# Kernel optimization log

Measured on AMD Instinct MI355X. Metric: run time of the kernel, lower is better.

The kernel has to match this reference:

```python
import jax, jax.numpy as jnp
import numpy as np

N_NODES = 100000
N_EDGES = 1600000
IN_DIM = 128
HIDDEN = 128


def setup_inputs() -> dict:
    key = jax.random.key(0)
    k1, k2, k3, k4 = jax.random.split(key, 4)
    x = jax.random.normal(k1, (N_NODES, IN_DIM), dtype=jnp.float32)
    edge_index = jax.random.randint(k2, (2, N_EDGES), 0, N_NODES, dtype=jnp.int32)
    # Glorot-ish scale (module zero-inits weights, which would give trivial
    # outputs; use random weights for a meaningful correctness baseline).
    W1 = jax.random.normal(k3, (IN_DIM, HIDDEN), dtype=jnp.float32) * (1.0 / np.sqrt(IN_DIM))
    W2 = jax.random.normal(k4, (HIDDEN, HIDDEN), dtype=jnp.float32) * (1.0 / np.sqrt(HIDDEN))
    return {"x": x, "edge_index": edge_index, "W1": W1, "W2": W2}


def _gcn_conv(h, W, src, dst, norm):
    # linear transform then normalized scatter-add aggregation (PyG GCNConv, bias=False)
    h = h @ W                              # [N, H]
    msg = h[src] * norm[:, None]           # gather + scale: [E+N, H]
    return jax.ops.segment_sum(msg, dst, num_segments=N_NODES)


def reference(x, edge_index, W1, W2):
    # add self-loops
    loops = jnp.arange(N_NODES, dtype=edge_index.dtype)
    src = jnp.concatenate([edge_index[0], loops])
    dst = jnp.concatenate([edge_index[1], loops])
    # symmetric normalization D^{-1/2} (A+I) D^{-1/2}; deg >= 1 due to self-loops
    deg = jax.ops.segment_sum(jnp.ones_like(dst, dtype=x.dtype), dst, num_segments=N_NODES)
    dinv = jax.lax.rsqrt(deg)
    norm = dinv[src] * dinv[dst]           # [E+N]

    h = _gcn_conv(x, W1, src, dst, norm)
    h = jax.nn.relu(h)                     # dropout is identity in eval mode
    h = _gcn_conv(h, W2, src, dst, norm)
    return h
```

## Files before the change

kernel.cpp:

```cpp
#include <hip/hip_runtime.h>
#include <hip/hip_bf16.h>

typedef unsigned short u16;
typedef unsigned int   u32;

typedef __attribute__((ext_vector_type(8))) short short8;
typedef __attribute__((ext_vector_type(4))) float floatx4;

#define HD __device__ __forceinline__

HD float bf16_lo(u32 u) { union { u32 i; float f; } v; v.i = u << 16; return v.f; }
HD float bf16_hi(u32 u) { union { u32 i; float f; } v; v.i = u & 0xffff0000u; return v.f; }
HD u16 f2bf(float f) {
    __hip_bfloat16 h = __float2bfloat16(f);
    u16 s; __builtin_memcpy(&s, &h, 2); return s;
}

#define NPB   256
#define MAXNB 512
#define CH    4096
#define CAP   5120

__global__ void k_wprep(const u32* __restrict__ xw,
                        const void* __restrict__ W1, const void* __restrict__ W2,
                        u16* __restrict__ W1t, u16* __restrict__ W2t,
                        int* __restrict__ flag, int* __restrict__ gbcursor) {
    __shared__ int cnt;
    if (threadIdx.x == 0) cnt = 0;
    __syncthreads();
    int sane = 0;
    for (int i = threadIdx.x; i < 4096; i += 256) {
        u32 v = xw[i];
        int e = (v >> 7) & 0xFF;
        sane += (e >= 107 && e <= 147) ? 1 : 0;
    }
    atomicAdd(&cnt, sane);
    __syncthreads();
    int isbf = (cnt > 2048) ? 1 : 0;
    if (blockIdx.x == 0) {
        if (threadIdx.x == 0) *flag = isbf;
        for (int i = threadIdx.x; i <= MAXNB; i += 256) gbcursor[i] = i * CAP;
    }
    int i = blockIdx.x * blockDim.x + threadIdx.x;
    int w = i >> 14;
    int r = (i >> 7) & 127;
    int c = i & 127;
    const void* W = w ? W2 : W1;
    u16*       Wt = w ? W2t : W1t;
    u16 val;
    if (isbf) val = ((const u16*)W)[c * 128 + r];
    else      val = f2bf(((const float*)W)[c * 128 + r]);
    Wt[r * 128 + c] = val;
}

template <int MODE>
__device__ __forceinline__
void gemm_body(u16* __restrict__ lw, u16* __restrict__ st_all,
               const void* __restrict__ inp, const u16* __restrict__ Wt,
               u16* __restrict__ outb, int ntiles, int isbf, int gw, int nw) {
    int lane = threadIdx.x & 63;
    int wid  = threadIdx.x >> 6;
    int m = lane & 15, q = lane >> 4;
    u16* st = st_all + wid * (16 * 136);

    {
        int r = threadIdx.x >> 1;
        int h = threadIdx.x & 1;
        const short8* src = (const short8*)(Wt + r * 128 + h * 64);
#pragma unroll
        for (int jj = 0; jj < 8; jj++) {
            int slot = h * 8 + jj;
            *(short8*)&lw[r * 128 + ((slot ^ (r & 7)) << 3)] = src[jj];
        }
    }
    __syncthreads();

    for (int t = gw; t < ntiles; t += nw) {
        long r0 = (long)t * 32;
        floatx4 acc[2][8];
#pragma unroll
        for (int g = 0; g < 2; g++)
#pragma unroll
            for (int nt = 0; nt < 8; nt++) acc[g][nt] = (floatx4)0.0f;

        short8 a[2][4];
        if (MODE == 1 || isbf) {
#pragma unroll
            for (int g = 0; g < 2; g++)
#pragma unroll
                for (int kk = 0; kk < 4; kk++)
                    a[g][kk] = *(const short8*)((const u16*)inp +
                                 (r0 + g * 16 + m) * 128 + kk * 32 + q * 8);
        } else {
#pragma unroll
            for (int g = 0; g < 2; g++)
#pragma unroll
                for (int kk = 0; kk < 4; kk++) {
                    const float4* fp = (const float4*)((const float*)inp +
                                 (r0 + g * 16 + m) * 128 + kk * 32 + q * 8);
                    float4 f0 = fp[0], f1 = fp[1];
                    short8 v;
                    v[0] = (short)f2bf(f0.x); v[1] = (short)f2bf(f0.y);
                    v[2] = (short)f2bf(f0.z); v[3] = (short)f2bf(f0.w);
                    v[4] = (short)f2bf(f1.x); v[5] = (short)f2bf(f1.y);
                    v[6] = (short)f2bf(f1.z); v[7] = (short)f2bf(f1.w);
                    a[g][kk] = v;
                }
        }

#pragma unroll
        for (int kk = 0; kk < 4; kk++) {
#pragma unroll
            for (int nt = 0; nt < 8; nt++) {
                int slot = kk * 4 + q;
                short8 b = *(const short8*)&lw[(nt * 16 + m) * 128 +
                                               ((slot ^ (m & 7)) << 3)];
                acc[0][nt] = __builtin_amdgcn_mfma_f32_16x16x32_bf16(a[0][kk], b, acc[0][nt], 0, 0, 0);
                acc[1][nt] = __builtin_amdgcn_mfma_f32_16x16x32_bf16(a[1][kk], b, acc[1][nt], 0, 0, 0);
            }
        }

#pragma unroll
        for (int g = 0; g < 2; g++) {
#pragma unroll
            for (int nt = 0; nt < 8; nt++)
#pragma unroll
                for (int i = 0; i < 4; i++)
                    st[(q * 4 + i) * 136 + nt * 16 + m] = f2bf(acc[g][nt][i]);
            __builtin_amdgcn_s_waitcnt(0);
            u16* gbase = outb + (size_t)(r0 + g * 16) * 128;
#pragma unroll
            for (int j = 0; j < 4; j++) {
                int e   = lane * 8 + j * 512;
                int row = e >> 7, colu = e & 127;
                short8 vv = *(const short8*)&st[row * 136 + colu];
                *(short8*)(gbase + e) = vv;
            }
            __builtin_amdgcn_s_waitcnt(0);
        }
    }
}

__device__ __forceinline__
void coarse_body(char* smem, const int* __restrict__ ei, int* __restrict__ gbcursor,
                 int2* __restrict__ pairs, int E, int chunk) {
    int*  hist = (int*)smem;
    int*  gs   = hist + MAXNB;
    int*  dlt  = gs + MAXNB;
    int*  lofs = dlt + MAXNB;
    int2* lp   = (int2*)(smem + 8192);
    u16*  pb   = (u16*)(smem + 8192 + CH * 8);
    const int* srcp = ei;
    const int* dstp = ei + E;
    int base = chunk * CH;
    int cnt  = min(CH, E - base);

    for (int i = threadIdx.x; i < MAXNB; i += 256) hist[i] = 0;
    __syncthreads();

    int2 e[16];
    int nb_ = 0;
#pragma unroll
    for (int j = 0; j < 16; j++) {
        int i = base + threadIdx.x + j * 256;
        if (i < E) {
            e[j].x = srcp[i];
            e[j].y = dstp[i];
            atomicAdd(&hist[e[j].y >> 8], 1);
            nb_ = j + 1;
        }
    }
    __syncthreads();

    if (threadIdx.x < 64) {
        int lane = threadIdx.x;
        int carry = 0;
#pragma unroll
        for (int t = 0; t < MAXNB / 64; t++) {
            int i = t * 64 + lane;
            int v = hist[i];
            int x = v;
#pragma unroll
            for (int off = 1; off < 64; off <<= 1) {
                int y = __shfl_up(x, off);
                if (lane >= off) x += y;
            }
            gs[i] = carry + x - v;
            carry += __shfl(x, 63);
        }
    }
    __syncthreads();

    for (int b = threadIdx.x; b < MAXNB; b += 256) {
        int c = hist[b];
        lofs[b] = gs[b];
        if (c > 0) {
            int gbase = atomicAdd(&gbcursor[b], c);
            dlt[b] = gbase - gs[b];
        }
    }
    __syncthreads();

    for (int j = 0; j < nb_; j++) {
        int b = e[j].y >> 8;
        int p = atomicAdd(&lofs[b], 1);
        lp[p] = e[j];
        pb[p] = (u16)b;
    }
    __syncthreads();

    for (int p = threadIdx.x; p < cnt; p += 256) {
        pairs[p + dlt[pb[p]]] = lp[p];
    }
}

__global__ void __launch_bounds__(256)
k_fused1(const void* __restrict__ x, const u16* __restrict__ W1t,
         u16* __restrict__ Hb, int ntiles, const int* __restrict__ flagp,
         const int* __restrict__ ei, int* __restrict__ gbcursor,
         int2* __restrict__ pairs, int E, int gemmBlocks) {
    __shared__ __align__(16) char smem[50176];
    if (blockIdx.x < gemmBlocks) {
        int isbf = *flagp;
        int gw = (blockIdx.x * 256 + threadIdx.x) >> 6;
        int nw = gemmBlocks * 4;
        gemm_body<0>((u16*)smem, (u16*)(smem + 32768), x, W1t, Hb, ntiles, isbf, gw, nw);
    } else {
        coarse_body(smem, ei, gbcursor, pairs, E, blockIdx.x - gemmBlocks);
    }
}

__global__ void __launch_bounds__(256)
k_gemm2(const void* __restrict__ inp, const u16* __restrict__ Wt,
        u16* __restrict__ outb, int ntiles) {
    __shared__ u16 lw[128 * 128];
    __shared__ u16 stage[4][16 * 136];
    int gw = (blockIdx.x * 256 + threadIdx.x) >> 6;
    int nw = (gridDim.x * 256) >> 6;
    gemm_body<1>(lw, &stage[0][0], inp, Wt, outb, ntiles, 1, gw, nw);
}

__global__ void __launch_bounds__(256)
k_bucket(const int2* __restrict__ pairs, const int* __restrict__ gbcursor,
         float* __restrict__ dinv, int* __restrict__ rbeg, int* __restrict__ rend,
         int* __restrict__ col, int N) {
    __shared__ int lc[NPB];
    __shared__ int lcur[NPB];
    __shared__ int ws[4];
    __shared__ int wsoff[4];
    int b = blockIdx.x;
    int nbase = b * NPB;
    int tid = threadIdx.x, lane = tid & 63, wid = tid >> 6;
    lc[tid] = 0;
    __syncthreads();
    int p0 = b * CAP, p1 = gbcursor[b];
    for (int p = p0 + tid; p < p1; p += 256)
        atomicAdd(&lc[pairs[p].y - nbase], 1);
    __syncthreads();
    int v = lc[tid];
    int node = nbase + tid;
    if (node < N) dinv[node] = rsqrtf((float)v + 1.0f);
    int x = v;
#pragma unroll
    for (int off = 1; off < 64; off <<= 1) {
        int y = __shfl_up(x, off);
        if (lane >= off) x += y;
    }
    if (lane == 63) ws[wid] = x;
    __syncthreads();
    if (tid == 0) {
        int s = 0;
#pragma unroll
        for (int k2 = 0; k2 < 4; k2++) { wsoff[k2] = s; s += ws[k2]; }
    }
    __syncthreads();
    int excl = p0 + wsoff[wid] + (x - v);
    if (node < N) { rbeg[node] = excl; rend[node] = excl + v; }
    lcur[tid] = excl;
    __syncthreads();
    for (int p = p0 + tid; p < p1; p += 256) {
        int2 e = pairs[p];
        int pos = atomicAdd(&lcur[e.y - nbase], 1);
        col[pos] = e.x;
    }
}

template <int MODE>
__global__ void k_csr_agg(const u16* __restrict__ Hb, const int* __restrict__ col,
                          const int* __restrict__ rbeg, const int* __restrict__ rend,
                          const float* __restrict__ dinv,
                          void* __restrict__ outp, int N, const int* __restrict__ flagp) {
    int isbf = MODE ? *flagp : 1;
    int gw   = (blockIdx.x * blockDim.x + threadIdx.x) >> 6;
    int nw   = (gridDim.x * blockDim.x) >> 6;
    int lane = threadIdx.x & 63;
    const u16* hbl = Hb + lane * 2;
    for (int n = gw; n < N; n += nw) {
        int r0 = rbeg[n], r1 = rend[n];
        float di = dinv[n];
        u32 h = *(const u32*)(hbl + (size_t)n * 128);
        float a0 = bf16_lo(h) * di, a1 = bf16_hi(h) * di;

        for (int base = r0; base < r1; base += 64) {
            int cnt = min(64, r1 - base);
            int   myc = (lane < cnt) ? col[base + lane] : 0;
            float mdv = (lane < cnt) ? dinv[myc] : 0.0f;
            int e = 0;
            for (; e + 15 < cnt; e += 16) {
                u32 hh[16]; float cf[16];
#pragma unroll
                for (int j = 0; j < 16; j++) {
                    int s = __builtin_amdgcn_readlane(myc, e + j);
                    cf[j] = __int_as_float(__builtin_amdgcn_readlane(__float_as_int(mdv), e + j));
                    hh[j] = *(const u32*)(hbl + (size_t)s * 128);
                }
#pragma unroll
                for (int j = 0; j < 16; j++) {
                    a0 += bf16_lo(hh[j]) * cf[j];
                    a1 += bf16_hi(hh[j]) * cf[j];
                }
            }
            for (; e + 7 < cnt; e += 8) {
                u32 hh[8]; float cf[8];
#pragma unroll
                for (int j = 0; j < 8; j++) {
                    int s = __builtin_amdgcn_readlane(myc, e + j);
                    cf[j] = __int_as_float(__builtin_amdgcn_readlane(__float_as_int(mdv), e + j));
                    hh[j] = *(const u32*)(hbl + (size_t)s * 128);
                }
#pragma unroll
                for (int j = 0; j < 8; j++) {
                    a0 += bf16_lo(hh[j]) * cf[j];
                    a1 += bf16_hi(hh[j]) * cf[j];
                }
            }
            for (; e + 3 < cnt; e += 4) {
                u32 hh[4]; float cf[4];
#pragma unroll
                for (int j = 0; j < 4; j++) {
                    int s = __builtin_amdgcn_readlane(myc, e + j);
                    cf[j] = __int_as_float(__builtin_amdgcn_readlane(__float_as_int(mdv), e + j));
                    hh[j] = *(const u32*)(hbl + (size_t)s * 128);
                }
#pragma unroll
                for (int j = 0; j < 4; j++) {
                    a0 += bf16_lo(hh[j]) * cf[j];
                    a1 += bf16_hi(hh[j]) * cf[j];
                }
            }
            for (; e < cnt; e++) {
                int   s  = __builtin_amdgcn_readlane(myc, e);
                float cf = __int_as_float(__builtin_amdgcn_readlane(__float_as_int(mdv), e));
                u32  hh  = *(const u32*)(hbl + (size_t)s * 128);
                a0 += bf16_lo(hh) * cf; a1 += bf16_hi(hh) * cf;
            }
        }

        a0 *= di; a1 *= di;

        if (MODE == 0) {
            float r0f = fmaxf(a0, 0.0f), r1f = fmaxf(a1, 0.0f);
            ((u32*)outp)[(size_t)n * 64 + lane] = (u32)f2bf(r0f) | ((u32)f2bf(r1f) << 16);
        } else if (isbf) {
            ((u32*)outp)[(size_t)n * 64 + lane] = (u32)f2bf(a0) | ((u32)f2bf(a1) << 16);
        } else {
            ((float2*)outp)[(size_t)n * 64 + lane] = make_float2(a0, a1);
        }
    }
}

extern "C" void kernel_launch(void* const* d_in, const int* in_sizes, int n_in,
                              void* d_out, int out_size, void* d_ws, size_t ws_size,
                              hipStream_t stream) {
    const void* x  = d_in[0];
    const int*  ei = (const int*)d_in[1];
    const void* W1 = d_in[2];
    const void* W2 = d_in[3];

    const int N = in_sizes[0] / 128;
    const int E = in_sizes[1] / 2;

    char* ws = (char*)d_ws;
    float* dinv    = (float*)ws;
    int*   rbeg    = (int*)(ws + (512u << 10));
    int*   rend    = (int*)(ws + (1024u << 10));
    int*   gbcur   = (int*)(ws + (1536u << 10));
    int*   flag    = (int*)(ws + (1600u << 10));
    u16*   W1t     = (u16*)(ws + (2048u << 10));
    u16*   W2t     = W1t + 128 * 128;
    int*   col     = (int*)(ws + (3u << 20));
    u16*   Hb      = (u16*)(ws + (12u << 20));
    u16*   A       = (u16*)(ws + (38u << 20));
    int2*  pairs   = (int2*)(ws + (64u << 20));

    int NB  = (N + NPB - 1) / NPB;
    int nch = (E + CH - 1) / CH;

    int ntiles     = N / 32;
    int gemmBlocks = (ntiles + 3) / 4;
    int ablocks    = (N + 3) / 4;

    k_wprep<<<128, 256, 0, stream>>>((const u32*)x, W1, W2, W1t, W2t, flag, gbcur);
    k_fused1<<<gemmBlocks + nch, 256, 0, stream>>>(x, W1t, Hb, ntiles, flag,
                                                   ei, gbcur, pairs, E, gemmBlocks);
    k_bucket<<<NB, 256, 0, stream>>>(pairs, gbcur, dinv, rbeg, rend, col, N);

    k_csr_agg<0><<<ablocks, 256, 0, stream>>>(Hb, col, rbeg, rend, dinv, A, N, flag);

    k_gemm2<<<gemmBlocks, 256, 0, stream>>>(A, W2t, Hb, ntiles);
    k_csr_agg<1><<<ablocks, 256, 0, stream>>>(Hb, col, rbeg, rend, dinv, d_out, N, flag);
}
```

Measured before the change: 307.6 us.

## Fuse first-layer aggregation with second GEMM and widen bucket kernel to 512 threads

The layer-1 CSR aggregation, ReLU and the W2 GEMM are merged into one kernel. Each block aggregates 32 nodes into shared memory as bf16 and multiplies them by W2 with MFMA, so the intermediate activation never round-trips through global memory and one launch disappears. The bucket kernel now runs with 512 threads so its pair-scanning loops take larger strides. The risk is that the fused kernel only launches about 3125 blocks with 8 nodes per wave handled serially, which may hide gather latency less well than the old one-node-per-wave layout.

```diff
diff --git a/kernel.cpp b/kernel.cpp
--- a/kernel.cpp
+++ b/kernel.cpp
@@ -230,17 +230,7 @@
     }
 }
 
-__global__ void __launch_bounds__(256)
-k_gemm2(const void* __restrict__ inp, const u16* __restrict__ Wt,
-        u16* __restrict__ outb, int ntiles) {
-    __shared__ u16 lw[128 * 128];
-    __shared__ u16 stage[4][16 * 136];
-    int gw = (blockIdx.x * 256 + threadIdx.x) >> 6;
-    int nw = (gridDim.x * 256) >> 6;
-    gemm_body<1>(lw, &stage[0][0], inp, Wt, outb, ntiles, 1, gw, nw);
-}
-
-__global__ void __launch_bounds__(256)
+__global__ void __launch_bounds__(512)
 k_bucket(const int2* __restrict__ pairs, const int* __restrict__ gbcursor,
          float* __restrict__ dinv, int* __restrict__ rbeg, int* __restrict__ rend,
          int* __restrict__ col, int N) {
@@ -251,22 +241,24 @@
     int b = blockIdx.x;
     int nbase = b * NPB;
     int tid = threadIdx.x, lane = tid & 63, wid = tid >> 6;
-    lc[tid] = 0;
+    if (tid < NPB) lc[tid] = 0;
     __syncthreads();
     int p0 = b * CAP, p1 = gbcursor[b];
-    for (int p = p0 + tid; p < p1; p += 256)
+    for (int p = p0 + tid; p < p1; p += 512)
         atomicAdd(&lc[pairs[p].y - nbase], 1);
     __syncthreads();
-    int v = lc[tid];
-    int node = nbase + tid;
-    if (node < N) dinv[node] = rsqrtf((float)v + 1.0f);
-    int x = v;
-#pragma unroll
-    for (int off = 1; off < 64; off <<= 1) {
-        int y = __shfl_up(x, off);
-        if (lane >= off) x += y;
-    }
-    if (lane == 63) ws[wid] = x;
+    int v = 0, x = 0, node = nbase + tid;
+    if (tid < NPB) {
+        v = lc[tid];
+        if (node < N) dinv[node] = rsqrtf((float)v + 1.0f);
+        x = v;
+#pragma unroll
+        for (int off = 1; off < 64; off <<= 1) {
+            int y = __shfl_up(x, off);
+            if (lane >= off) x += y;
+        }
+        if (lane == 63) ws[wid] = x;
+    }
     __syncthreads();
     if (tid == 0) {
         int s = 0;
@@ -274,94 +266,165 @@
         for (int k2 = 0; k2 < 4; k2++) { wsoff[k2] = s; s += ws[k2]; }
     }
     __syncthreads();
-    int excl = p0 + wsoff[wid] + (x - v);
-    if (node < N) { rbeg[node] = excl; rend[node] = excl + v; }
-    lcur[tid] = excl;
-    __syncthreads();
-    for (int p = p0 + tid; p < p1; p += 256) {
+    if (tid < NPB) {
+        int excl = p0 + wsoff[wid] + (x - v);
+        if (node < N) { rbeg[node] = excl; rend[node] = excl + v; }
+        lcur[tid] = excl;
+    }
+    __syncthreads();
+    for (int p = p0 + tid; p < p1; p += 512) {
         int2 e = pairs[p];
         int pos = atomicAdd(&lcur[e.y - nbase], 1);
         col[pos] = e.x;
     }
 }
 
-template <int MODE>
-__global__ void k_csr_agg(const u16* __restrict__ Hb, const int* __restrict__ col,
-                          const int* __restrict__ rbeg, const int* __restrict__ rend,
-                          const float* __restrict__ dinv,
-                          void* __restrict__ outp, int N, const int* __restrict__ flagp) {
-    int isbf = MODE ? *flagp : 1;
+HD void agg_node(const u16* __restrict__ hbl, const int* __restrict__ col,
+                 const float* __restrict__ dinv, int r0, int r1, int n,
+                 float di, int lane, float& a0o, float& a1o) {
+    u32 h = *(const u32*)(hbl + (size_t)n * 128);
+    float a0 = bf16_lo(h) * di, a1 = bf16_hi(h) * di;
+    for (int base = r0; base < r1; base += 64) {
+        int cnt = min(64, r1 - base);
+        int   myc = (lane < cnt) ? col[base + lane] : 0;
+        float mdv = (lane < cnt) ? dinv[myc] : 0.0f;
+        int e = 0;
+        for (; e + 15 < cnt; e += 16) {
+            u32 hh[16]; float cf[16];
+#pragma unroll
+            for (int j = 0; j < 16; j++) {
+                int s = __builtin_amdgcn_readlane(myc, e + j);
+                cf[j] = __int_as_float(__builtin_amdgcn_readlane(__float_as_int(mdv), e + j));
+                hh[j] = *(const u32*)(hbl + (size_t)s * 128);
+            }
+#pragma unroll
+            for (int j = 0; j < 16; j++) {
+                a0 += bf16_lo(hh[j]) * cf[j];
+                a1 += bf16_hi(hh[j]) * cf[j];
+            }
+        }
+        for (; e + 7 < cnt; e += 8) {
+            u32 hh[8]; float cf[8];
+#pragma unroll
+            for (int j = 0; j < 8; j++) {
+                int s = __builtin_amdgcn_readlane(myc, e + j);
+                cf[j] = __int_as_float(__builtin_amdgcn_readlane(__float_as_int(mdv), e + j));
+                hh[j] = *(const u32*)(hbl + (size_t)s * 128);
+            }
+#pragma unroll
+            for (int j = 0; j < 8; j++) {
+                a0 += bf16_lo(hh[j]) * cf[j];
+                a1 += bf16_hi(hh[j]) * cf[j];
+            }
+        }
+        for (; e + 3 < cnt; e += 4) {
+            u32 hh[4]; float cf[4];
+#pragma unroll
+            for (int j = 0; j < 4; j++) {
+                int s = __builtin_amdgcn_readlane(myc, e + j);
+                cf[j] = __int_as_float(__builtin_amdgcn_readlane(__float_as_int(mdv), e + j));
+                hh[j] = *(const u32*)(hbl + (size_t)s * 128);
+            }
+#pragma unroll
+            for (int j = 0; j < 4; j++) {
+                a0 += bf16_lo(hh[j]) * cf[j];
+                a1 += bf16_hi(hh[j]) * cf[j];
+            }
+        }
+        for (; e < cnt; e++) {
+            int   s  = __builtin_amdgcn_readlane(myc, e);
+            float cf = __int_as_float(__builtin_amdgcn_readlane(__float_as_int(mdv), e));
+            u32  hh  = *(const u32*)(hbl + (size_t)s * 128);
+            a0 += bf16_lo(hh) * cf; a1 += bf16_hi(hh) * cf;
+        }
+    }
+    a0o = a0 * di; a1o = a1 * di;
+}
+
+__global__ void __launch_bounds__(256)
+k_aggemm(const u16* __restrict__ Hb, const int* __restrict__ col,
+         const int* __restrict__ rbeg, const int* __restrict__ rend,
+         const float* __restrict__ dinv, const u16* __restrict__ W2t,
+         u16* __restrict__ Hb2, int N) {
+    __shared__ u32 arow[32 * 68];
+    int tid  = threadIdx.x;
+    int lane = tid & 63, wid = tid >> 6;
+    int m = lane & 15, q = lane >> 4;
+    int nbase = blockIdx.x * 32;
+
+    short8 bfr[2][4];
+#pragma unroll
+    for (int ntl = 0; ntl < 2; ntl++)
+#pragma unroll
+        for (int kk = 0; kk < 4; kk++)
+            bfr[ntl][kk] = *(const short8*)(W2t + ((wid * 2 + ntl) * 16 + m) * 128 +
+                                            kk * 32 + q * 8);
+
+    const u16* hbl = Hb + lane * 2;
+    for (int k = 0; k < 8; k++) {
+        int r = wid * 8 + k;
+        int n = nbase + r;
+        float a0 = 0.0f, a1 = 0.0f;
+        if (n < N) {
+            agg_node(hbl, col, dinv, rbeg[n], rend[n], n, dinv[n], lane, a0, a1);
+        }
+        float r0f = fmaxf(a0, 0.0f), r1f = fmaxf(a1, 0.0f);
+        arow[r * 68 + lane] = (u32)f2bf(r0f) | ((u32)f2bf(r1f) << 16);
+    }
+    __syncthreads();
+
+    const u16* ar16 = (const u16*)arow;
+    floatx4 acc[2][2];
+#pragma unroll
+    for (int g = 0; g < 2; g++)
+#pragma unroll
+        for (int ntl = 0; ntl < 2; ntl++) acc[g][ntl] = (floatx4)0.0f;
+#pragma unroll
+    for (int g = 0; g < 2; g++) {
+#pragma unroll
+        for (int kk = 0; kk < 4; kk++) {
+            short8 a = *(const short8*)(ar16 + (g * 16 + m) * 136 + kk * 32 + q * 8);
+            acc[g][0] = __builtin_amdgcn_mfma_f32_16x16x32_bf16(a, bfr[0][kk], acc[g][0], 0, 0, 0);
+            acc[g][1] = __builtin_amdgcn_mfma_f32_16x16x32_bf16(a, bfr[1][kk], acc[g][1], 0, 0, 0);
+        }
+    }
+    __syncthreads();
+
+    u16* st = (u16*)arow;
+#pragma unroll
+    for (int g = 0; g < 2; g++)
+#pragma unroll
+        for (int ntl = 0; ntl < 2; ntl++)
+#pragma unroll
+            for (int i = 0; i < 4; i++)
+                st[(g * 16 + q * 4 + i) * 136 + (wid * 2 + ntl) * 16 + m] = f2bf(acc[g][ntl][i]);
+    __syncthreads();
+
+    u16* gbase = Hb2 + (size_t)nbase * 128;
+#pragma unroll
+    for (int j = 0; j < 2; j++) {
+        int e   = tid * 8 + j * 2048;
+        int row = e >> 7, colu = e & 127;
+        if (nbase + row < N) {
+            short8 vv = *(const short8*)&st[row * 136 + colu];
+            *(short8*)(gbase + e) = vv;
+        }
+    }
+}
+
+__global__ void k_csr_agg2(const u16* __restrict__ Hb, const int* __restrict__ col,
+                           const int* __restrict__ rbeg, const int* __restrict__ rend,
+                           const float* __restrict__ dinv,
+                           void* __restrict__ outp, int N, const int* __restrict__ flagp) {
+    int isbf = *flagp;
     int gw   = (blockIdx.x * blockDim.x + threadIdx.x) >> 6;
     int nw   = (gridDim.x * blockDim.x) >> 6;
     int lane = threadIdx.x & 63;
     const u16* hbl = Hb + lane * 2;
     for (int n = gw; n < N; n += nw) {
-        int r0 = rbeg[n], r1 = rend[n];
-        float di = dinv[n];
-        u32 h = *(const u32*)(hbl + (size_t)n * 128);
-        float a0 = bf16_lo(h) * di, a1 = bf16_hi(h) * di;
-
-        for (int base = r0; base < r1; base += 64) {
-            int cnt = min(64, r1 - base);
-            int   myc = (lane < cnt) ? col[base + lane] : 0;
-            float mdv = (lane < cnt) ? dinv[myc] : 0.0f;
-            int e = 0;
-            for (; e + 15 < cnt; e += 16) {
-                u32 hh[16]; float cf[16];
-#pragma unroll
-                for (int j = 0; j < 16; j++) {
-                    int s = __builtin_amdgcn_readlane(myc, e + j);
-                    cf[j] = __int_as_float(__builtin_amdgcn_readlane(__float_as_int(mdv), e + j));
-                    hh[j] = *(const u32*)(hbl + (size_t)s * 128);
-                }
-#pragma unroll
-                for (int j = 0; j < 16; j++) {
-                    a0 += bf16_lo(hh[j]) * cf[j];
-                    a1 += bf16_hi(hh[j]) * cf[j];
-                }
-            }
-            for (; e + 7 < cnt; e += 8) {
-                u32 hh[8]; float cf[8];
-#pragma unroll
-                for (int j = 0; j < 8; j++) {
-                    int s = __builtin_amdgcn_readlane(myc, e + j);
-                    cf[j] = __int_as_float(__builtin_amdgcn_readlane(__float_as_int(mdv), e + j));
-                    hh[j] = *(const u32*)(hbl + (size_t)s * 128);
-                }
-#pragma unroll
-                for (int j = 0; j < 8; j++) {
-                    a0 += bf16_lo(hh[j]) * cf[j];
-                    a1 += bf16_hi(hh[j]) * cf[j];
-                }
-            }
-            for (; e + 3 < cnt; e += 4) {
-                u32 hh[4]; float cf[4];
-#pragma unroll
-                for (int j = 0; j < 4; j++) {
-                    int s = __builtin_amdgcn_readlane(myc, e + j);
-                    cf[j] = __int_as_float(__builtin_amdgcn_readlane(__float_as_int(mdv), e + j));
-                    hh[j] = *(const u32*)(hbl + (size_t)s * 128);
-                }
-#pragma unroll
-                for (int j = 0; j < 4; j++) {
-                    a0 += bf16_lo(hh[j]) * cf[j];
-                    a1 += bf16_hi(hh[j]) * cf[j];
-                }
-            }
-            for (; e < cnt; e++) {
-                int   s  = __builtin_amdgcn_readlane(myc, e);
-                float cf = __int_as_float(__builtin_amdgcn_readlane(__float_as_int(mdv), e));
-                u32  hh  = *(const u32*)(hbl + (size_t)s * 128);
-                a0 += bf16_lo(hh) * cf; a1 += bf16_hi(hh) * cf;
-            }
-        }
-
-        a0 *= di; a1 *= di;
-
-        if (MODE == 0) {
-            float r0f = fmaxf(a0, 0.0f), r1f = fmaxf(a1, 0.0f);
-            ((u32*)outp)[(size_t)n * 64 + lane] = (u32)f2bf(r0f) | ((u32)f2bf(r1f) << 16);
-        } else if (isbf) {
+        float a0, a1;
+        agg_node(hbl, col, dinv, rbeg[n], rend[n], n, dinv[n], lane, a0, a1);
+        if (isbf) {
             ((u32*)outp)[(size_t)n * 64 + lane] = (u32)f2bf(a0) | ((u32)f2bf(a1) << 16);
         } else {
             ((float2*)outp)[(size_t)n * 64 + lane] = make_float2(a0, a1);
@@ -390,7 +453,7 @@
     u16*   W2t     = W1t + 128 * 128;
     int*   col     = (int*)(ws + (3u << 20));
     u16*   Hb      = (u16*)(ws + (12u << 20));
-    u16*   A       = (u16*)(ws + (38u << 20));
+    u16*   Hb2     = (u16*)(ws + (38u << 20));
     int2*  pairs   = (int2*)(ws + (64u << 20));
 
     int NB  = (N + NPB - 1) / NPB;
@@ -399,14 +462,14 @@
     int ntiles     = N / 32;
     int gemmBlocks = (ntiles + 3) / 4;
     int ablocks    = (N + 3) / 4;
+    int fblocks    = (N + 31) / 32;
 
     k_wprep<<<128, 256, 0, stream>>>((const u32*)x, W1, W2, W1t, W2t, flag, gbcur);
     k_fused1<<<gemmBlocks + nch, 256, 0, stream>>>(x, W1t, Hb, ntiles, flag,
                                                    ei, gbcur, pairs, E, gemmBlocks);
-    k_bucket<<<NB, 256, 0, stream>>>(pairs, gbcur, dinv, rbeg, rend, col, N);
-
-    k_csr_agg<0><<<ablocks, 256, 0, stream>>>(Hb, col, rbeg, rend, dinv, A, N, flag);
-
-    k_gemm2<<<gemmBlocks, 256, 0, stream>>>(A, W2t, Hb, ntiles);
-    k_csr_agg<1><<<ablocks, 256, 0, stream>>>(Hb, col, rbeg, rend, dinv, d_out, N, flag);
-}
+    k_bucket<<<NB, 512, 0, stream>>>(pairs, gbcur, dinv, rbeg, rend, col, N);
+
+    k_aggemm<<<fblocks, 256, 0, stream>>>(Hb, col, rbeg, rend, dinv, W2t, Hb2, N);
+
+    k_csr_agg2<<<ablocks, 256, 0, stream>>>(Hb2, col, rbeg, rend, dinv, d_out, N, flag);
+}
```

New measurement: 324.0 us. 1.05x slower.
